# Performance work log

Hardware: AMD Instinct MI355X
Metric: run time of the kernel (lower is better)

## Reference

```python
import jax, jax.numpy as jnp
import numpy as np

B, N, D, H, L = 16, 512, 256, 8, 4
DK = D // H
EPS_LN = 1e-6
EPS_ADJ = 1e-6
NEG_INF = -1e12
LAM_ATT, LAM_DIST, LAM_ADJ = 0.3, 0.3, 0.4
SLOPE = 0.1  # leaky_relu_slope


def setup_inputs() -> dict:
    key = jax.random.key(0)
    ks = jax.random.split(key, 24)
    s = 1.0 / np.sqrt(D)
    w = lambda k: jax.random.normal(k, (L, D, D), jnp.float32) * s
    b = lambda k: jax.random.normal(k, (L, D), jnp.float32) * 0.01
    return {
        "x": jax.random.normal(ks[0], (B, N, D), jnp.float32),
        "mask": jax.random.randint(ks[1], (B, N), 0, 2, jnp.int32),
        "adj_matrix": jax.random.uniform(ks[2], (B, N, N), jnp.float32),
        "distance_matrix": jax.random.uniform(ks[3], (B, N, N), jnp.float32) * 10.0,
        "edges_att": jnp.zeros((1,), jnp.float32),  # unused (use_edge_features=False)
        "Wq": w(ks[4]), "bq": b(ks[5]),
        "Wk": w(ks[6]), "bk": b(ks[7]),
        "Wv": w(ks[8]), "bv": b(ks[9]),
        "Wo": w(ks[10]), "bo": b(ks[11]),
        "Wf1": w(ks[12]), "bf1": b(ks[13]),
        "Wf2": w(ks[14]), "bf2": b(ks[15]),
        "ln1_a": jnp.ones((L, D), jnp.float32), "ln1_b": jnp.zeros((L, D), jnp.float32),
        "ln2_a": jnp.ones((L, D), jnp.float32), "ln2_b": jnp.zeros((L, D), jnp.float32),
        "lnf_a": jnp.ones((D,), jnp.float32), "lnf_b": jnp.zeros((D,), jnp.float32),
    }


def _layernorm(x, a, b):
    # torch LayerNorm here uses unbiased std and divides by (std + eps)
    m = x.mean(-1, keepdims=True)
    s = jnp.std(x, axis=-1, ddof=1, keepdims=True)
    return a * (x - m) / (s + EPS_LN) + b


def reference(x, mask, adj_matrix, distance_matrix, edges_att,
              Wq, bq, Wk, bk, Wv, bv, Wo, bo, Wf1, bf1, Wf2, bf2,
              ln1_a, ln1_b, ln2_a, ln2_b, lnf_a, lnf_b):
    maskk = (mask != 0)[:, None, :]                      # [B,1,N] key mask
    # distance kernel: softmax(-dist) with masked keys -> weight 0
    p_dist = jax.nn.softmax(jnp.where(maskk, -distance_matrix, -jnp.inf), axis=-1)  # [B,N,N]
    # row-normalized adjacency
    p_adj = adj_matrix / (adj_matrix.sum(-1, keepdims=True) + EPS_ADJ)              # [B,N,N]
    mk4 = maskk[:, :, None, :]                           # [B,1,1,N]
    inv_sqrt_dk = 1.0 / np.sqrt(DK)

    for i in range(L):
        # --- self-attention sublayer (pre-norm residual) ---
        h_in = _layernorm(x, ln1_a[i], ln1_b[i])
        q = (h_in @ Wq[i] + bq[i]).reshape(B, N, H, DK).transpose(0, 2, 1, 3)
        k = (h_in @ Wk[i] + bk[i]).reshape(B, N, H, DK).transpose(0, 2, 1, 3)
        v = (h_in @ Wv[i] + bv[i]).reshape(B, N, H, DK).transpose(0, 2, 1, 3)
        scores = jnp.einsum('bhqd,bhkd->bhqk', q, k) * inv_sqrt_dk
        p_attn = jax.nn.softmax(jnp.where(mk4, scores, NEG_INF), axis=-1)
        # three-way fused weighting over [B,H,N,N]
        p = LAM_ATT * p_attn + LAM_DIST * p_dist[:, None] + LAM_ADJ * p_adj[:, None]
        att = jnp.einsum('bhqk,bhkd->bhqd', p, v).transpose(0, 2, 1, 3).reshape(B, N, D)
        x = x + (att @ Wo[i] + bo[i])
        # --- FFN sublayer (pre-norm residual), N_dense=2 with leaky_relu ---
        h2 = _layernorm(x, ln2_a[i], ln2_b[i])
        h2 = jax.nn.leaky_relu(h2 @ Wf1[i] + bf1[i], negative_slope=SLOPE)
        h2 = jax.nn.leaky_relu(h2 @ Wf2[i] + bf2[i], negative_slope=SLOPE)
        x = x + h2

    return _layernorm(x, lnf_a, lnf_b)
```

## Files before the change

### kernel.cpp

```cpp
#include <hip/hip_runtime.h>
#include <hip/hip_bf16.h>
#include <math.h>

constexpr int kB  = 16;
constexpr int kN  = 512;
constexpr int kD  = 256;
constexpr int kH  = 8;
constexpr int kDK = 32;
constexpr int kL  = 4;

using bf16 = __hip_bfloat16;
using short8 = __attribute__((ext_vector_type(8))) short;
using floatx4 = __attribute__((ext_vector_type(4))) float;

__device__ __forceinline__ float fast_exp2(float x) {
#if __has_builtin(__builtin_amdgcn_exp2f)
    return __builtin_amdgcn_exp2f(x);
#else
    return __expf(x * 0.69314718055994531f);
#endif
}

__device__ __forceinline__ float bfs2f(short s) {
    unsigned u = ((unsigned)(unsigned short)s) << 16;
    return __uint_as_float(u);
}

__device__ __forceinline__ void gl2lds16(const bf16* g, bf16* s) {
    __builtin_amdgcn_global_load_lds(
        (const __attribute__((address_space(1))) void*)g,
        (__attribute__((address_space(3))) void*)s, 16, 0, 0);
}

__device__ __forceinline__ int swzA(int row, int inrow_byte) {
    return row * 512 + (inrow_byte ^ ((row & 7) << 4));
}

__device__ __forceinline__ float blockReduceSum(float v, float* sh) {
    #pragma unroll
    for (int o = 32; o > 0; o >>= 1) v += __shfl_down(v, o, 64);
    int lane = threadIdx.x & 63, w = threadIdx.x >> 6;
    __syncthreads();
    if (lane == 0) sh[w] = v;
    __syncthreads();
    return sh[0] + sh[1] + sh[2] + sh[3];
}

__device__ __forceinline__ float blockReduceMax(float v, float* sh) {
    #pragma unroll
    for (int o = 32; o > 0; o >>= 1) v = fmaxf(v, __shfl_down(v, o, 64));
    int lane = threadIdx.x & 63, w = threadIdx.x >> 6;
    __syncthreads();
    if (lane == 0) sh[w] = v;
    __syncthreads();
    return fmaxf(fmaxf(sh[0], sh[1]), fmaxf(sh[2], sh[3]));
}

__global__ __launch_bounds__(256) void prep_kernel(const float* __restrict__ Wq,
                                                   const float* __restrict__ Wk,
                                                   const float* __restrict__ Wv,
                                                   const float* __restrict__ Wo,
                                                   const float* __restrict__ Wf1,
                                                   const float* __restrict__ Wf2,
                                                   const float* __restrict__ bq,
                                                   const float* __restrict__ bk,
                                                   const float* __restrict__ bv,
                                                   const float* __restrict__ adj,
                                                   const float* __restrict__ dist,
                                                   const int* __restrict__ mask,
                                                   const float* __restrict__ x,
                                                   const float* __restrict__ ln1a,
                                                   const float* __restrict__ ln1b,
                                                   bf16* __restrict__ wqkv,
                                                   bf16* __restrict__ wo,
                                                   bf16* __restrict__ wf1,
                                                   bf16* __restrict__ wf2,
                                                   float* __restrict__ bcat,
                                                   bf16* __restrict__ pcb,
                                                   bf16* __restrict__ h) {
    __shared__ float tile[32][33];
    __shared__ float sh[4];
    int bid = blockIdx.x;
    int t = threadIdx.x;

    if (bid < 1536) {
        int mat = bid >> 6;
        int t6 = bid & 63;
        int tr = t6 >> 3, tc = t6 & 7;
        int layer = mat / 6, slot = mat % 6;
        const float* src =
            slot == 0 ? Wq : slot == 1 ? Wk : slot == 2 ? Wv :
            slot == 3 ? Wo : slot == 4 ? Wf1 : Wf2;
        src += (size_t)layer * kD * kD;
        bf16* dst;
        if (slot < 3) dst = wqkv + ((size_t)layer * 768 + slot * 256) * kD;
        else dst = (slot == 3 ? wo : slot == 4 ? wf1 : wf2) + (size_t)layer * kD * kD;
        int r = t >> 5, c = t & 31;
        #pragma unroll
        for (int i = 0; i < 4; i++)
            tile[r + i * 8][c] = src[(size_t)(tr * 32 + r + i * 8) * kD + tc * 32 + c];
        __syncthreads();
        #pragma unroll
        for (int i = 0; i < 4; i++)
            dst[(size_t)(tc * 32 + r + i * 8) * kD + tr * 32 + c] = bf16(tile[c][r + i * 8]);
    } else if (bid < 1548) {
        int idx = (bid - 1536) * 256 + t;
        int layer = idx / 768, j = idx % 768;
        const float* s = j < 256 ? bq : j < 512 ? bk : bv;
        bcat[idx] = s[layer * 256 + (j & 255)];
    } else if (bid < 1548 + kB * kN) {
        int row = bid - 1548;
        int b = row >> 9;
        const float* dr = dist + (size_t)row * kN;
        const float* ar = adj + (size_t)row * kN;
        const int* mr = mask + b * kN;
        float d0 = dr[t], d1 = dr[t + 256];
        float a0 = ar[t], a1 = ar[t + 256];
        int m0 = mr[t], m1 = mr[t + 256];
        const float kLog2e = 1.4426950408889634f;
        float s0 = m0 ? -d0 * kLog2e : -INFINITY;
        float s1 = m1 ? -d1 * kLog2e : -INFINITY;
        float mx = blockReduceMax(fmaxf(s0, s1), sh);
        float e0 = fast_exp2(s0 - mx);
        float e1 = fast_exp2(s1 - mx);
        float sum  = blockReduceSum(e0 + e1, sh);
        float asum = blockReduceSum(a0 + a1, sh);
        float w_d = 0.3f / sum;
        float w_a = 0.4f / (asum + 1e-6f);
        bf16* pr = pcb + (size_t)row * kN;
        pr[t]       = bf16(e0 * w_d + a0 * w_a);
        pr[t + 256] = bf16(e1 * w_d + a1 * w_a);
    } else {
        int row = bid - (1548 + kB * kN);
        float v = x[(size_t)row * kD + t];
        float m = blockReduceSum(v, sh) * (1.0f / kD);
        float dd = v - m;
        float var = blockReduceSum(dd * dd, sh) * (1.0f / (kD - 1));
        float s = sqrtf(var);
        h[(size_t)row * kD + t] = bf16(ln1a[t] * dd / (s + 1e-6f) + ln1b[t]);
    }
}

__global__ __launch_bounds__(256) void gemm_qkv(const bf16* __restrict__ A,
                                                const bf16* __restrict__ Wt,
                                                const float* __restrict__ bias,
                                                bf16* __restrict__ Cv) {
    __shared__ __align__(16) bf16 As[2][128][32];
    __shared__ __align__(16) bf16 Bs[2][64][32];
    int t = threadIdx.x;
    int m0 = blockIdx.x * 128, n0 = blockIdx.y * 64;
    int lane = t & 63, w = t >> 6, g = lane >> 4, li = lane & 15;
    int sr = lane >> 2;
    int sc = (lane & 3) * 8;

    const bf16* aSrc0 = A + (size_t)(m0 + w * 32 + sr) * kD + sc;
    const bf16* aSrc1 = aSrc0 + (size_t)16 * kD;
    const bf16* bSrc  = Wt + (size_t)(n0 + w * 16 + sr) * kD + sc;

    floatx4 zero = {0.f, 0.f, 0.f, 0.f};
    floatx4 acc[2][4];
    #pragma unroll
    for (int i = 0; i < 2; i++)
        #pragma unroll
        for (int j = 0; j < 4; j++) acc[i][j] = zero;

    auto stage = [&](int buf, int k0) {
        gl2lds16(aSrc0 + k0, &As[buf][w * 32][0]);
        gl2lds16(aSrc1 + k0, &As[buf][w * 32 + 16][0]);
        gl2lds16(bSrc  + k0, &Bs[buf][w * 16][0]);
    };

    stage(0, 0);
    __syncthreads();

    #pragma unroll
    for (int ks = 0; ks < 8; ks++) {
        const int cur = ks & 1;
        if (ks < 7) stage(cur ^ 1, (ks + 1) * 32);
        short8 af0 = *(const short8*)&As[cur][w * 32 + li][g * 8];
        short8 af1 = *(const short8*)&As[cur][w * 32 + 16 + li][g * 8];
        #pragma unroll
        for (int ct = 0; ct < 4; ct++) {
            short8 bfr = *(const short8*)&Bs[cur][ct * 16 + li][g * 8];
            acc[0][ct] = __builtin_amdgcn_mfma_f32_16x16x32_bf16(af0, bfr, acc[0][ct], 0, 0, 0);
            acc[1][ct] = __builtin_amdgcn_mfma_f32_16x16x32_bf16(af1, bfr, acc[1][ct], 0, 0, 0);
        }
        if (ks < 7) __syncthreads();
    }

    #pragma unroll
    for (int rt = 0; rt < 2; rt++) {
        #pragma unroll
        for (int ct = 0; ct < 4; ct++) {
            #pragma unroll
            for (int rr = 0; rr < 4; rr++) {
                int m = m0 + w * 32 + rt * 16 + g * 4 + rr;
                int n = n0 + ct * 16 + li;
                float v = acc[rt][ct][rr] + bias[n];
                int j = n >> 8, nn = n & 255;
                int b = m >> 9, nr = m & 511;
                int hh = nn >> 5, dk = nn & 31;
                Cv[(size_t)j * (kB * kN * kD) +
                   (((size_t)(b * kH + hh)) * kN + nr) * kDK + dk] = bf16(v);
            }
        }
    }
}

__global__ __launch_bounds__(256, 2) void attn_mfma(const bf16* __restrict__ qb,
                                                    const bf16* __restrict__ kb,
                                                    const bf16* __restrict__ vb,
                                                    const bf16* __restrict__ pcb,
                                                    const int* __restrict__ mask,
                                                    bf16* __restrict__ att) {
    __shared__ __align__(16) bf16 Vf[16 * 2 * 64 * 8];
    __shared__ __align__(16) bf16 Pbuf[4][16][136];

    int blk = blockIdx.x;
    int qt = blk & 7;
    int bh = blk >> 3;
    int b = bh >> 3;
    int h = bh & 7;
    int t = threadIdx.x;
    int lane = t & 63, w = t >> 6;
    int g = lane >> 4, li = lane & 15;

    {
        const float4* vsrc4 = (const float4*)(vb + (size_t)bh * kN * kDK);
        #pragma unroll
        for (int it = 0; it < 8; it++) {
            int idx = t + it * 256;
            float4 raw = vsrc4[idx];
            union { float4 f; bf16 hh[8]; } u; u.f = raw;
            int f0 = idx * 8;
            int n = f0 >> 5, dk0 = f0 & 31;
            int kt = n >> 5, j = n & 7, gsl = (n >> 3) & 3;
            #pragma unroll
            for (int e = 0; e < 8; e++) {
                int dk = dk0 + e;
                int dt = dk >> 4;
                int lsl = (gsl << 4) | (dk & 15);
                Vf[((((kt << 1) | dt) << 6) | lsl) * 8 + j] = u.hh[e];
            }
        }
    }
    __syncthreads();

    const bf16* qrow = qb + ((size_t)bh * kN + qt * 64 + w * 16 + li) * kDK + g * 8;
    short8 aQ = *(const short8*)qrow;
    const bf16* kbase = kb + (size_t)bh * kN * kDK;
    const int* mb = mask + b * kN;
    unsigned mbits = 0;
    #pragma unroll
    for (int tt = 0; tt < 32; tt++)
        mbits |= (unsigned)(mb[tt * 16 + li] != 0) << tt;

    floatx4 s[32];
    floatx4 zero = {0.f, 0.f, 0.f, 0.f};
    #pragma unroll
    for (int tt = 0; tt < 32; tt++) {
        short8 bK = *(const short8*)(kbase + (size_t)(tt * 16 + li) * kDK + g * 8);
        s[tt] = __builtin_amdgcn_mfma_f32_16x16x32_bf16(aQ, bK, zero, 0, 0, 0);
    }

    const float scale = 0.17677669529663689f * 1.4426950408889634f;
    #pragma unroll
    for (int r = 0; r < 4; r++) {
        float sum = 0.f;
        #pragma unroll
        for (int tt = 0; tt < 32; tt++) {
            bool mm = (mbits >> tt) & 1;
            float e = mm ? fast_exp2(s[tt][r] * scale) : 0.f;
            s[tt][r] = e;
            sum += e;
        }
        #pragma unroll
        for (int o = 1; o < 16; o <<= 1) sum += __shfl_xor(sum, o, 64);
        float inv = 0.3f / sum;
        #pragma unroll
        for (int tt = 0; tt < 32; tt++) s[tt][r] *= inv;
    }

    {
        const short* pcq = (const short*)(pcb + ((size_t)b * kN + qt * 64 + w * 16) * kN);
        #pragma unroll
        for (int tt = 0; tt < 32; tt++) {
            #pragma unroll
            for (int r = 0; r < 4; r++)
                s[tt][r] += bfs2f(pcq[(size_t)(g * 4 + r) * kN + tt * 16 + li]);
        }
    }

    bf16* pb = &Pbuf[w][0][0];
    floatx4 accA0 = zero, accA1 = zero;
    #pragma unroll
    for (int c = 0; c < 4; c++) {
        #pragma unroll
        for (int ttl = 0; ttl < 8; ttl++) {
            int tt = c * 8 + ttl;
            int kcol = ttl * 16 + li;
            #pragma unroll
            for (int r = 0; r < 4; r++)
                pb[(g * 4 + r) * 136 + kcol] = bf16(s[tt][r]);
        }
        #pragma unroll
        for (int k2 = 0; k2 < 4; k2++) {
            int ktile = c * 4 + k2;
            short8 aP  = *(const short8*)(pb + li * 136 + k2 * 32 + g * 8);
            short8 bV0 = *(const short8*)(&Vf[((ktile * 2 + 0) * 64 + lane) * 8]);
            short8 bV1 = *(const short8*)(&Vf[((ktile * 2 + 1) * 64 + lane) * 8]);
            accA0 = __builtin_amdgcn_mfma_f32_16x16x32_bf16(aP, bV0, accA0, 0, 0, 0);
            accA1 = __builtin_amdgcn_mfma_f32_16x16x32_bf16(aP, bV1, accA1, 0, 0, 0);
        }
    }

    #pragma unroll
    for (int r = 0; r < 4; r++) {
        size_t row = (size_t)b * kN + qt * 64 + w * 16 + g * 4 + r;
        bf16* arow = att + row * kD + h * kDK;
        arow[li]      = bf16(accA0[r]);
        arow[16 + li] = bf16(accA1[r]);
    }
}

__device__ __forceinline__ void gemm_phase16(const char* asb, const bf16* __restrict__ Wt,
                                             bf16 (*Bs)[256][32],
                                             int w, int lane, int g, int li,
                                             floatx4 acc[4]) {
    auto stageB = [&](int buf, int k0) {
        #pragma unroll
        for (int c = 0; c < 4; c++) {
            int row = w * 64 + c * 16;
            gl2lds16(Wt + (size_t)(row + (lane >> 2)) * kD + k0 + (lane & 3) * 8,
                     &Bs[buf][row][0]);
        }
    };
    stageB(0, 0);
    #pragma unroll
    for (int ks = 0; ks < 8; ks++) {
        const int cur = ks & 1;
        __builtin_amdgcn_sched_barrier(0);
        if (ks < 7) {
            stageB(cur ^ 1, (ks + 1) * 32);
            asm volatile("s_waitcnt vmcnt(4)" ::: "memory");
        } else {
            asm volatile("s_waitcnt vmcnt(0)" ::: "memory");
        }
        __builtin_amdgcn_sched_barrier(0);
        short8 af0 = *(const short8*)(asb + swzA(li, (ks * 4 + g) << 4));
        #pragma unroll
        for (int ct = 0; ct < 4; ct++) {
            short8 bfr = *(const short8*)&Bs[cur][w * 64 + ct * 16 + li][g * 8];
            acc[ct] = __builtin_amdgcn_mfma_f32_16x16x32_bf16(af0, bfr, acc[ct], 0, 0, 0);
        }
    }
}

__device__ __forceinline__ void row_ln_stats16(floatx4 xv[4],
                                               float (*psumS)[16], float (*psqS)[16],
                                               int w, int g, int li,
                                               float outMean[4], float outInv[4]) {
    #pragma unroll
    for (int rr = 0; rr < 4; rr++) {
        float s4 = 0.f, q4 = 0.f;
        #pragma unroll
        for (int ct = 0; ct < 4; ct++) {
            float v = xv[ct][rr];
            s4 += v;
            q4 += v * v;
        }
        #pragma unroll
        for (int o = 1; o < 16; o <<= 1) {
            s4 += __shfl_xor(s4, o, 64);
            q4 += __shfl_xor(q4, o, 64);
        }
        int row = g * 4 + rr;
        if (li == 0) { psumS[w][row] = s4; psqS[w][row] = q4; }
    }
    __syncthreads();
    #pragma unroll
    for (int rr = 0; rr < 4; rr++) {
        int row = g * 4 + rr;
        float s  = psumS[0][row] + psumS[1][row] + psumS[2][row] + psumS[3][row];
        float ss = psqS[0][row]  + psqS[1][row]  + psqS[2][row]  + psqS[3][row];
        float mean = s * (1.0f / kD);
        float var = (ss - (float)kD * mean * mean) * (1.0f / (kD - 1));
        outMean[rr] = mean;
        outInv[rr] = 1.0f / (sqrtf(var) + 1e-6f);
    }
}

template <bool LAST>
__global__ __launch_bounds__(256) void block_tail(const bf16* __restrict__ A,
                                                  const bf16* __restrict__ Wot,
                                                  const float* __restrict__ bo,
                                                  const float* __restrict__ resid,
                                                  const bf16* __restrict__ W1t,
                                                  const float* __restrict__ b1,
                                                  const bf16* __restrict__ W2t,
                                                  const float* __restrict__ b2,
                                                  const float* __restrict__ ln2a,
                                                  const float* __restrict__ ln2b,
                                                  const float* __restrict__ lnna,
                                                  const float* __restrict__ lnnb,
                                                  float* __restrict__ xcOut,
                                                  bf16* __restrict__ hOut,
                                                  float* __restrict__ fOut) {
    __shared__ __align__(16) bf16 As[16][256];
    __shared__ __align__(16) bf16 Bs[2][256][32];
    __shared__ float psumS[4][16], psqS[4][16];

    int t = threadIdx.x;
    int m0 = blockIdx.x * 16;
    int lane = t & 63, w = t >> 6, g = lane >> 4, li = lane & 15;

    {
        int r = t >> 4;
        int cbase = (t & 15) * 2;
        const bf16* src = A + (size_t)(m0 + r) * kD;
        char* asb = (char*)&As[0][0];
        #pragma unroll
        for (int c = 0; c < 2; c++) {
            int chunk = cbase + c;
            short8 v = *(const short8*)(src + chunk * 8);
            *(short8*)(asb + swzA(r, chunk << 4)) = v;
        }
    }
    __syncthreads();

    floatx4 zero = {0.f, 0.f, 0.f, 0.f};
    floatx4 acc[4];
    #pragma unroll
    for (int j = 0; j < 4; j++) acc[j] = zero;

    gemm_phase16((const char*)&As[0][0], Wot, Bs, w, lane, g, li, acc);

    floatx4 xs[4];
    #pragma unroll
    for (int ct = 0; ct < 4; ct++) {
        #pragma unroll
        for (int rr = 0; rr < 4; rr++) {
            int m = m0 + g * 4 + rr;
            int n = w * 64 + ct * 16 + li;
            float xv = resid[(size_t)m * kD + n] + acc[ct][rr] + bo[n];
            xs[ct][rr] = xv;
            acc[ct][rr] = xv;
        }
    }

    float mean[4], inv[4];
    row_ln_stats16(acc, psumS, psqS, w, g, li, mean, inv);
    {
        char* asb = (char*)&As[0][0];
        #pragma unroll
        for (int ct = 0; ct < 4; ct++) {
            #pragma unroll
            for (int rr = 0; rr < 4; rr++) {
                int row = g * 4 + rr;
                int col = w * 64 + ct * 16 + li;
                float y = ln2a[col] * (xs[ct][rr] - mean[rr]) * inv[rr] + ln2b[col];
                *(bf16*)(asb + swzA(row, col * 2)) = bf16(y);
            }
        }
    }
    __syncthreads();

    #pragma unroll
    for (int j = 0; j < 4; j++) acc[j] = zero;

    gemm_phase16((const char*)&As[0][0], W1t, Bs, w, lane, g, li, acc);

    __syncthreads();

    {
        char* asb = (char*)&As[0][0];
        #pragma unroll
        for (int ct = 0; ct < 4; ct++) {
            #pragma unroll
            for (int rr = 0; rr < 4; rr++) {
                int row = g * 4 + rr;
                int col = w * 64 + ct * 16 + li;
                float v = acc[ct][rr] + b1[col];
                v = v > 0.f ? v : 0.1f * v;
                *(bf16*)(asb + swzA(row, col * 2)) = bf16(v);
            }
        }
    }
    __syncthreads();

    #pragma unroll
    for (int j = 0; j < 4; j++) acc[j] = zero;

    gemm_phase16((const char*)&As[0][0], W2t, Bs, w, lane, g, li, acc);

    #pragma unroll
    for (int ct = 0; ct < 4; ct++) {
        #pragma unroll
        for (int rr = 0; rr < 4; rr++) {
            int m = m0 + g * 4 + rr;
            int n = w * 64 + ct * 16 + li;
            float v = acc[ct][rr] + b2[n];
            v = v > 0.f ? v : 0.1f * v;
            float xv = xs[ct][rr] + v;
            if (!LAST) xcOut[(size_t)m * kD + n] = xv;
            acc[ct][rr] = xv;
        }
    }

    row_ln_stats16(acc, psumS, psqS, w, g, li, mean, inv);

    #pragma unroll
    for (int ct = 0; ct < 4; ct++) {
        #pragma unroll
        for (int rr = 0; rr < 4; rr++) {
            int m = m0 + g * 4 + rr;
            int n = w * 64 + ct * 16 + li;
            float y = lnna[n] * (acc[ct][rr] - mean[rr]) * inv[rr] + lnnb[n];
            if (LAST) fOut[(size_t)m * kD + n] = y;
            else      hOut[(size_t)m * kD + n] = bf16(y);
        }
    }
}

extern "C" void kernel_launch(void* const* d_in, const int* in_sizes, int n_in,
                              void* d_out, int out_size, void* d_ws, size_t ws_size,
                              hipStream_t stream) {
    const float* x    = (const float*)d_in[0];
    const int*   mask = (const int*)d_in[1];
    const float* adj  = (const float*)d_in[2];
    const float* dist = (const float*)d_in[3];
    const float* Wq = (const float*)d_in[5];  const float* bq = (const float*)d_in[6];
    const float* Wk = (const float*)d_in[7];  const float* bk = (const float*)d_in[8];
    const float* Wv = (const float*)d_in[9];  const float* bv = (const float*)d_in[10];
    const float* Wo = (const float*)d_in[11]; const float* bo = (const float*)d_in[12];
    const float* Wf1 = (const float*)d_in[13]; const float* bf1 = (const float*)d_in[14];
    const float* Wf2 = (const float*)d_in[15]; const float* bf2 = (const float*)d_in[16];
    const float* ln1a = (const float*)d_in[17]; const float* ln1b = (const float*)d_in[18];
    const float* ln2a = (const float*)d_in[19]; const float* ln2b = (const float*)d_in[20];
    const float* lnfa = (const float*)d_in[21]; const float* lnfb = (const float*)d_in[22];

    const size_t rows = (size_t)kB * kN;
    const size_t actN = rows * kD;

    char* wsb = (char*)d_ws;
    bf16*  pcb   = (bf16*)wsb;  wsb += (size_t)kB * kN * kN * sizeof(bf16);
    float* xc    = (float*)wsb; wsb += actN * sizeof(float);
    bf16*  h     = (bf16*)wsb;  wsb += actN * sizeof(bf16);
    bf16*  attb  = (bf16*)wsb;  wsb += actN * sizeof(bf16);
    bf16*  qkvb  = (bf16*)wsb;  wsb += 3 * actN * sizeof(bf16);
    bf16*  wqkv  = (bf16*)wsb;  wsb += (size_t)kL * 768 * kD * sizeof(bf16);
    bf16*  wo_t  = (bf16*)wsb;  wsb += (size_t)kL * kD * kD * sizeof(bf16);
    bf16*  wf1_t = (bf16*)wsb;  wsb += (size_t)kL * kD * kD * sizeof(bf16);
    bf16*  wf2_t = (bf16*)wsb;  wsb += (size_t)kL * kD * kD * sizeof(bf16);
    float* bcat  = (float*)wsb; wsb += (size_t)kL * 768 * sizeof(float);

    prep_kernel<<<1548 + 2 * kB * kN, 256, 0, stream>>>(
        Wq, Wk, Wv, Wo, Wf1, Wf2, bq, bk, bv, adj, dist, mask, x, ln1a, ln1b,
        wqkv, wo_t, wf1_t, wf2_t, bcat, pcb, h);

    dim3 gQKV(64, 12);
    const int g16 = rows / 16;
    for (int i = 0; i < kL; i++) {
        const size_t bOff = (size_t)i * kD;
        const size_t wOff = (size_t)i * kD * kD;
        const float* xin = (i == 0) ? x : xc;
        gemm_qkv<<<gQKV, 256, 0, stream>>>(h, wqkv + (size_t)i * 768 * kD,
                                           bcat + (size_t)i * 768, qkvb);
        attn_mfma<<<kB * kH * (kN / 64), 256, 0, stream>>>(qkvb, qkvb + actN,
                                                           qkvb + 2 * actN,
                                                           pcb, mask, attb);
        if (i < kL - 1) {
            block_tail<false><<<g16, 256, 0, stream>>>(
                attb, wo_t + wOff, bo + bOff, xin,
                wf1_t + wOff, bf1 + bOff, wf2_t + wOff, bf2 + bOff,
                ln2a + bOff, ln2b + bOff,
                ln1a + (size_t)(i + 1) * kD, ln1b + (size_t)(i + 1) * kD,
                xc, h, nullptr);
        } else {
            block_tail<true><<<g16, 256, 0, stream>>>(
                attb, wo_t + wOff, bo + bOff, xin,
                wf1_t + wOff, bf1 + bOff, wf2_t + wOff, bf2 + bOff,
                ln2a + bOff, ln2b + bOff, lnfa, lnfb,
                nullptr, nullptr, (float*)d_out);
        }
    }
}
```

Measured before the change: 353.1 us.

## Recompute QK scores in two passes to drop register array and raise occupancy

```diff
diff --git a/kernel.cpp b/kernel.cpp
--- a/kernel.cpp
+++ b/kernel.cpp
@@ -207,7 +207,7 @@
     }
 }
 
-__global__ __launch_bounds__(256, 2) void attn_mfma(const bf16* __restrict__ qb,
+__global__ __launch_bounds__(256, 3) void attn_mfma(const bf16* __restrict__ qb,
                                                     const bf16* __restrict__ kb,
                                                     const bf16* __restrict__ vb,
                                                     const bf16* __restrict__ pcb,
@@ -255,42 +255,29 @@
     for (int tt = 0; tt < 32; tt++)
         mbits |= (unsigned)(mb[tt * 16 + li] != 0) << tt;
 
-    floatx4 s[32];
     floatx4 zero = {0.f, 0.f, 0.f, 0.f};
+    const float scale = 0.17677669529663689f * 1.4426950408889634f;
+
+    float sums[4] = {0.f, 0.f, 0.f, 0.f};
     #pragma unroll
     for (int tt = 0; tt < 32; tt++) {
         short8 bK = *(const short8*)(kbase + (size_t)(tt * 16 + li) * kDK + g * 8);
-        s[tt] = __builtin_amdgcn_mfma_f32_16x16x32_bf16(aQ, bK, zero, 0, 0, 0);
-    }
-
-    const float scale = 0.17677669529663689f * 1.4426950408889634f;
+        floatx4 sv = __builtin_amdgcn_mfma_f32_16x16x32_bf16(aQ, bK, zero, 0, 0, 0);
+        bool mm = (mbits >> tt) & 1;
+        #pragma unroll
+        for (int r = 0; r < 4; r++)
+            sums[r] += mm ? fast_exp2(sv[r] * scale) : 0.f;
+    }
+    float inv[4];
     #pragma unroll
     for (int r = 0; r < 4; r++) {
-        float sum = 0.f;
-        #pragma unroll
-        for (int tt = 0; tt < 32; tt++) {
-            bool mm = (mbits >> tt) & 1;
-            float e = mm ? fast_exp2(s[tt][r] * scale) : 0.f;
-            s[tt][r] = e;
-            sum += e;
-        }
-        #pragma unroll
-        for (int o = 1; o < 16; o <<= 1) sum += __shfl_xor(sum, o, 64);
-        float inv = 0.3f / sum;
-        #pragma unroll
-        for (int tt = 0; tt < 32; tt++) s[tt][r] *= inv;
-    }
-
-    {
-        const short* pcq = (const short*)(pcb + ((size_t)b * kN + qt * 64 + w * 16) * kN);
-        #pragma unroll
-        for (int tt = 0; tt < 32; tt++) {
-            #pragma unroll
-            for (int r = 0; r < 4; r++)
-                s[tt][r] += bfs2f(pcq[(size_t)(g * 4 + r) * kN + tt * 16 + li]);
-        }
-    }
-
+        float s = sums[r];
+        #pragma unroll
+        for (int o = 1; o < 16; o <<= 1) s += __shfl_xor(s, o, 64);
+        inv[r] = 0.3f / s;
+    }
+
+    const short* pcq = (const short*)(pcb + ((size_t)b * kN + qt * 64 + w * 16) * kN);
     bf16* pb = &Pbuf[w][0][0];
     floatx4 accA0 = zero, accA1 = zero;
     #pragma unroll
@@ -298,10 +285,16 @@
         #pragma unroll
         for (int ttl = 0; ttl < 8; ttl++) {
             int tt = c * 8 + ttl;
+            short8 bK = *(const short8*)(kbase + (size_t)(tt * 16 + li) * kDK + g * 8);
+            floatx4 sv = __builtin_amdgcn_mfma_f32_16x16x32_bf16(aQ, bK, zero, 0, 0, 0);
+            bool mm = (mbits >> tt) & 1;
             int kcol = ttl * 16 + li;
             #pragma unroll
-            for (int r = 0; r < 4; r++)
-                pb[(g * 4 + r) * 136 + kcol] = bf16(s[tt][r]);
+            for (int r = 0; r < 4; r++) {
+                float p = mm ? fast_exp2(sv[r] * scale) * inv[r] : 0.f;
+                p += bfs2f(pcq[(size_t)(g * 4 + r) * kN + tt * 16 + li]);
+                pb[(g * 4 + r) * 136 + kcol] = bf16(p);
+            }
         }
         #pragma unroll
         for (int k2 = 0; k2 < 4; k2++) {
```

After: 372.9 us. 1.06x slower.
